# Kernel tuning notes

Hardware: AMD Instinct MI355X
Metric: run time of the kernel (lower is better)

Reference implementation:

```python
import math
import jax, jax.numpy as jnp
import numpy as np

DIM = 2048
NUM_HEADS = 16
HEAD_DIM = 128
SEQ = 2048
BATCH = 2
HIDDEN = 5632  # round_up(int(4*2048*2/3), 256)
EPS = 1e-6


def setup_inputs() -> dict:
    key = jax.random.key(0)
    ks = jax.random.split(key, 8)
    s = 0.02
    x = jax.random.normal(ks[0], (BATCH, SEQ, DIM), jnp.float32)
    wq = jax.random.normal(ks[1], (DIM, NUM_HEADS * HEAD_DIM), jnp.float32) * s
    wk = jax.random.normal(ks[2], (DIM, NUM_HEADS * HEAD_DIM), jnp.float32) * s
    wv = jax.random.normal(ks[3], (DIM, NUM_HEADS * HEAD_DIM), jnp.float32) * s
    wo = jax.random.normal(ks[4], (NUM_HEADS * HEAD_DIM, DIM), jnp.float32) * s
    w_mlp = jax.random.normal(ks[5], (HIDDEN, DIM), jnp.float32) * s
    v_mlp = jax.random.normal(ks[6], (HIDDEN, DIM), jnp.float32) * s
    w2_mlp = jax.random.normal(ks[7], (DIM, HIDDEN), jnp.float32) * s
    norm1_w = jnp.ones((DIM,), jnp.float32)
    norm2_w = jnp.ones((DIM,), jnp.float32)
    # RoPE tables: theta_i = 10000^{-2i/head_dim}, angle[p,i] = p * theta_i
    inv_freq = 1.0 / (10000.0 ** (np.arange(0, HEAD_DIM, 2, dtype=np.float32) / HEAD_DIM))
    angles = np.arange(SEQ, dtype=np.float32)[:, None] * inv_freq[None, :]  # [S, D/2]
    freqs_cos = jnp.asarray(np.cos(angles))
    freqs_sin = jnp.asarray(np.sin(angles))
    return {"x": x, "wq": wq, "wk": wk, "wv": wv, "wo": wo,
            "w_mlp": w_mlp, "v_mlp": v_mlp, "w2_mlp": w2_mlp,
            "norm1_w": norm1_w, "norm2_w": norm2_w,
            "freqs_cos": freqs_cos, "freqs_sin": freqs_sin}


def _rope(t, cos, sin):
    # t: [B,S,H,D] -> pairs, complex multiply by (cos + i sin)
    B, S, H, D = t.shape
    t = t.reshape(B, S, H, D // 2, 2)
    x0, x1 = t[..., 0], t[..., 1]
    c = cos[None, :S, None, :]
    s = sin[None, :S, None, :]
    o0 = x0 * c - x1 * s
    o1 = x0 * s + x1 * c
    return jnp.stack([o0, o1], axis=-1).reshape(B, S, H, D)


def _rmsnorm(x, w):
    x = x * jax.lax.rsqrt(jnp.mean(x * x, axis=-1, keepdims=True) + EPS)
    return w * x


def _attention(x, wq, wk, wv, wo, cos, sin):
    B, S, _ = x.shape
    q = (x @ wq).reshape(B, S, NUM_HEADS, HEAD_DIM)
    k = (x @ wk).reshape(B, S, NUM_HEADS, HEAD_DIM)
    v = (x @ wv).reshape(B, S, NUM_HEADS, HEAD_DIM)
    q = _rope(q, cos, sin)
    k = _rope(k, cos, sin)
    scores = jnp.einsum('bqhd,bkhd->bhqk', q, k) / math.sqrt(HEAD_DIM)
    causal = jnp.tril(jnp.ones((S, S), bool))
    scores = jnp.where(causal[None, None], scores, -jnp.inf)
    probs = jax.nn.softmax(scores.astype(jnp.float32), axis=-1)
    o = jnp.einsum('bhqk,bkhd->bqhd', probs, v).reshape(B, S, NUM_HEADS * HEAD_DIM)
    return o @ wo


def _mlp(x, w, v, w2):
    return (jax.nn.silu(x @ w.T) * (x @ v.T)) @ w2.T


def reference(x, wq, wk, wv, wo, w_mlp, v_mlp, w2_mlp, norm1_w, norm2_w, freqs_cos, freqs_sin):
    x = x + _attention(x, wq, wk, wv, wo, freqs_cos, freqs_sin)
    x = _rmsnorm(x, norm1_w)
    x = x + _mlp(x, w_mlp, v_mlp, w2_mlp)
    x = _rmsnorm(x, norm2_w)
    return x
```

## Files before the change

### kernel.cpp

```cpp
#include <hip/hip_runtime.h>

typedef unsigned short u16;
typedef unsigned int u32;
typedef float f32x4 __attribute__((ext_vector_type(4)));
typedef short bf16x8 __attribute__((ext_vector_type(8)));

#define DIM 2048
#define SEQ 2048
#define NHEAD 16
#define HDIM 128
#define BATCH 2
#define HIDDEN 5632
#define ROWS 4096

__device__ __forceinline__ float b2f(u16 h) { return __uint_as_float(((u32)h) << 16); }
__device__ __forceinline__ u16 f2b(float f) {
  u32 u = __float_as_uint(f);
  return (u16)((u + 0x7fffu + ((u >> 16) & 1u)) >> 16);
}

__global__ __launch_bounds__(256) void cvt_f2b(const float* __restrict__ in, u16* __restrict__ out, int n) {
  int i = (blockIdx.x * 256 + threadIdx.x) * 4;
  if (i < n) {
    float4 v = *(const float4*)(in + i);
    u32 p0 = (u32)f2b(v.x) | ((u32)f2b(v.y) << 16);
    u32 p1 = (u32)f2b(v.z) | ((u32)f2b(v.w) << 16);
    *(uint2*)(out + i) = make_uint2(p0, p1);
  }
}

__global__ __launch_bounds__(256) void cvtT(const float* __restrict__ in, u16* __restrict__ out,
                                            int Rr, int Cc) {
  __shared__ float t[32][33];
  int tx = threadIdx.x & 31, ty = threadIdx.x >> 5;
  int r0 = blockIdx.y * 32, c0 = blockIdx.x * 32;
#pragma unroll
  for (int rr = 0; rr < 4; ++rr)
    t[ty + rr * 8][tx] = in[(size_t)(r0 + ty + rr * 8) * Cc + c0 + tx];
  __syncthreads();
#pragma unroll
  for (int rr = 0; rr < 4; ++rr)
    out[(size_t)(c0 + ty + rr * 8) * Rr + r0 + tx] = f2b(t[tx][ty + rr * 8]);
}

__device__ __forceinline__ void stage_tile(u16* lds, const u16* __restrict__ g,
                                           int row0, int col0, int ld, int wave, int lane) {
#pragma unroll
  for (int j = 0; j < 2; ++j) {
    int i = wave * 2 + j;
    const u16* gp = g + (size_t)(row0 + i * 16 + (lane >> 2)) * ld + col0 + (lane & 3) * 8;
    __builtin_amdgcn_global_load_lds((const __attribute__((address_space(1))) void*)gp,
                                     (__attribute__((address_space(3))) void*)(lds + i * 512),
                                     16, 0, 0);
  }
}

template <int EPI>
__global__ __launch_bounds__(256) void gemm_bt(const u16* __restrict__ A, const u16* __restrict__ Bt,
                                               const void* R_, void* C_, int M, int N, int K) {
  __shared__ u16 lA[2][4096];
  __shared__ u16 lB[2][4096];
  const int tid = threadIdx.x, lane = tid & 63, wave = tid >> 6;
  const int wm = wave >> 1, wn = wave & 1;
  const int m0 = blockIdx.y * 128, n0 = blockIdx.x * 128;
  const int rl = lane & 15, g = lane >> 4;

  stage_tile(lA[0], A, m0, 0, K, wave, lane);
  stage_tile(lB[0], Bt, n0, 0, K, wave, lane);

  f32x4 acc[4][4];
#pragma unroll
  for (int a = 0; a < 4; ++a)
#pragma unroll
    for (int b = 0; b < 4; ++b) acc[a][b] = (f32x4){0.f, 0.f, 0.f, 0.f};

  __syncthreads();

  const int nk = K / 32;
  for (int kt = 0; kt < nk; ++kt) {
    const int cur = kt & 1;
    if (kt + 1 < nk) {
      stage_tile(lA[cur ^ 1], A, m0, (kt + 1) * 32, K, wave, lane);
      stage_tile(lB[cur ^ 1], Bt, n0, (kt + 1) * 32, K, wave, lane);
    }
    bf16x8 af[4], bfr[4];
#pragma unroll
    for (int mi = 0; mi < 4; ++mi)
      af[mi] = *reinterpret_cast<const bf16x8*>(&lA[cur][(wm * 64 + mi * 16 + rl) * 32 + g * 8]);
#pragma unroll
    for (int ni = 0; ni < 4; ++ni)
      bfr[ni] = *reinterpret_cast<const bf16x8*>(&lB[cur][(wn * 64 + ni * 16 + rl) * 32 + g * 8]);
#pragma unroll
    for (int mi = 0; mi < 4; ++mi)
#pragma unroll
      for (int ni = 0; ni < 4; ++ni)
        acc[mi][ni] = __builtin_amdgcn_mfma_f32_16x16x32_bf16(af[mi], bfr[ni], acc[mi][ni], 0, 0, 0);
    __syncthreads();
  }

#pragma unroll
  for (int mi = 0; mi < 4; ++mi)
#pragma unroll
    for (int ni = 0; ni < 4; ++ni)
#pragma unroll
      for (int j = 0; j < 4; ++j) {
        size_t row = m0 + wm * 64 + mi * 16 + g * 4 + j;
        size_t col = n0 + wn * 64 + ni * 16 + rl;
        size_t idx = row * N + col;
        float v = acc[mi][ni][j];
        if (EPI == 0) {
          ((u16*)C_)[idx] = f2b(v);
        } else if (EPI == 1) {
          ((float*)C_)[idx] = v + ((const float*)R_)[idx];
        } else if (EPI == 2) {
          float av = b2f(((const u16*)R_)[idx]);
          ((u16*)C_)[idx] = f2b(v * av / (1.f + __expf(-av)));
        } else {
          ((float*)C_)[idx] = v + b2f(((const u16*)R_)[idx]);
        }
      }
}

__global__ __launch_bounds__(256) void vtrans(const u16* __restrict__ V, u16* __restrict__ Vt) {
  __shared__ u16 t[32][33];
  int tx = threadIdx.x & 31, ty = threadIdx.x >> 5;
  int s0 = blockIdx.x * 32, d0 = blockIdx.y * 32;
  int bh = blockIdx.z, b = bh >> 4, h = bh & 15;
#pragma unroll
  for (int rr = 0; rr < 4; ++rr)
    t[ty + rr * 8][tx] = V[(size_t)(b * SEQ + s0 + ty + rr * 8) * DIM + h * HDIM + d0 + tx];
  __syncthreads();
#pragma unroll
  for (int rr = 0; rr < 4; ++rr)
    Vt[(size_t)(bh * HDIM + d0 + ty + rr * 8) * SEQ + s0 + tx] = t[tx][ty + rr * 8];
}

__global__ __launch_bounds__(256) void rope_kernel(u16* __restrict__ Q, u16* __restrict__ Kv,
                                                   const float* __restrict__ Cz, const float* __restrict__ Sz) {
  int t = blockIdx.x * 256 + threadIdx.x;
  int i = t & 63;
  int hh = (t >> 6) & 15;
  int row = t >> 10;
  int s = row & (SEQ - 1);
  float c = Cz[s * 64 + i], sn = Sz[s * 64 + i];
  size_t off = (size_t)row * DIM + hh * HDIM + 2 * i;
  const float sc = 0.08838834764831843f;

  u32 qp = *(const u32*)(Q + off);
  float q0 = b2f((u16)qp), q1 = b2f((u16)(qp >> 16));
  float o0 = (q0 * c - q1 * sn) * sc, o1 = (q0 * sn + q1 * c) * sc;
  *(u32*)(Q + off) = (u32)f2b(o0) | ((u32)f2b(o1) << 16);

  u32 kp = *(const u32*)(Kv + off);
  float k0 = b2f((u16)kp), k1 = b2f((u16)(kp >> 16));
  o0 = k0 * c - k1 * sn; o1 = k0 * sn + k1 * c;
  *(u32*)(Kv + off) = (u32)f2b(o0) | ((u32)f2b(o1) << 16);
}

__device__ __forceinline__ void attn_stage(u16* lk, u16* lv, const u16* __restrict__ Kg,
                                           const u16* __restrict__ Vg, int b, int h, int bh,
                                           int t, int w, int lane) {
#pragma unroll
  for (int j = 0; j < 4; ++j) {
    const u16* gp = Kg + (size_t)(b * SEQ + t * 64 + j * 16 + (lane >> 2)) * DIM +
                    h * HDIM + w * 32 + (lane & 3) * 8;
    __builtin_amdgcn_global_load_lds((const __attribute__((address_space(1))) void*)gp,
                                     (__attribute__((address_space(3))) void*)(lk + w * 2048 + j * 512),
                                     16, 0, 0);
  }
#pragma unroll
  for (int j = 0; j < 4; ++j) {
    int id = w * 4 + j, kc2 = id >> 3, rg = id & 7;
    const u16* gp = Vg + (size_t)(bh * HDIM + rg * 16 + (lane >> 2)) * SEQ +
                    t * 64 + kc2 * 32 + (lane & 3) * 8;
    __builtin_amdgcn_global_load_lds((const __attribute__((address_space(1))) void*)gp,
                                     (__attribute__((address_space(3))) void*)(lv + kc2 * 4096 + rg * 512),
                                     16, 0, 0);
  }
}

__device__ __forceinline__ void attn_tile(const bf16x8* qf, float* m, float* l, f32x4* oacc,
                                          int qg0, int t, bool diag,
                                          const u16* lk, const u16* lv, u16 (*pl)[72],
                                          int rl, int g) {
  f32x4 s[4];
#pragma unroll
  for (int ct = 0; ct < 4; ++ct) s[ct] = (f32x4){0.f, 0.f, 0.f, 0.f};
#pragma unroll
  for (int ct = 0; ct < 4; ++ct)
#pragma unroll
    for (int kc = 0; kc < 4; ++kc) {
      bf16x8 kf = *reinterpret_cast<const bf16x8*>(&lk[kc * 2048 + (ct * 16 + rl) * 32 + g * 8]);
      s[ct] = __builtin_amdgcn_mfma_f32_16x16x32_bf16(qf[kc], kf, s[ct], 0, 0, 0);
    }
  if (diag) {
#pragma unroll
    for (int ct = 0; ct < 4; ++ct) {
      int kg = t * 64 + ct * 16 + rl;
#pragma unroll
      for (int j = 0; j < 4; ++j)
        if (kg > qg0 + j) s[ct][j] = -1e30f;
    }
  }
  float mx[4], al[4];
#pragma unroll
  for (int j = 0; j < 4; ++j)
    mx[j] = fmaxf(fmaxf(s[0][j], s[1][j]), fmaxf(s[2][j], s[3][j]));
#pragma unroll
  for (int off = 1; off < 16; off <<= 1)
#pragma unroll
    for (int j = 0; j < 4; ++j) mx[j] = fmaxf(mx[j], __shfl_xor(mx[j], off));
#pragma unroll
  for (int j = 0; j < 4; ++j) {
    float mn = fmaxf(m[j], mx[j]);
    al[j] = __expf(m[j] - mn);
    m[j] = mn;
  }
  float rs[4] = {0.f, 0.f, 0.f, 0.f};
#pragma unroll
  for (int ct = 0; ct < 4; ++ct)
#pragma unroll
    for (int j = 0; j < 4; ++j) {
      float p = __expf(s[ct][j] - m[j]);
      s[ct][j] = p;
      rs[j] += p;
    }
#pragma unroll
  for (int off = 1; off < 16; off <<= 1)
#pragma unroll
    for (int j = 0; j < 4; ++j) rs[j] += __shfl_xor(rs[j], off);
#pragma unroll
  for (int j = 0; j < 4; ++j) l[j] = l[j] * al[j] + rs[j];
#pragma unroll
  for (int dt = 0; dt < 8; ++dt)
#pragma unroll
    for (int j = 0; j < 4; ++j) oacc[dt][j] *= al[j];

#pragma unroll
  for (int ct = 0; ct < 4; ++ct)
#pragma unroll
    for (int j = 0; j < 4; ++j) pl[g * 4 + j][ct * 16 + rl] = f2b(s[ct][j]);

  bf16x8 pa[2];
#pragma unroll
  for (int kc2 = 0; kc2 < 2; ++kc2)
    pa[kc2] = *reinterpret_cast<const bf16x8*>(&pl[rl][kc2 * 32 + g * 8]);

#pragma unroll
  for (int dt = 0; dt < 8; ++dt)
#pragma unroll
    for (int kc2 = 0; kc2 < 2; ++kc2) {
      bf16x8 vf = *reinterpret_cast<const bf16x8*>(&lv[kc2 * 4096 + (dt * 16 + rl) * 32 + g * 8]);
      oacc[dt] = __builtin_amdgcn_mfma_f32_16x16x32_bf16(pa[kc2], vf, oacc[dt], 0, 0, 0);
    }
}

__global__ __launch_bounds__(256) void attn_kernel(const u16* __restrict__ Q, const u16* __restrict__ Kp,
                                                   const u16* __restrict__ Vt, u16* __restrict__ O) {
  const int lane = threadIdx.x & 63;
  const int w = threadIdx.x >> 6;
  const int qa = blockIdx.x;
  const int qb = 31 - qa;
  const int bh = blockIdx.y;
  const int b = bh >> 4, h = bh & 15;
  const int rl = lane & 15, g = lane >> 4;

  __shared__ u16 lK[2][8192];
  __shared__ u16 lV[2][8192];
  __shared__ u16 plds[4][16][72];

  const size_t qrowA = (size_t)b * SEQ + qa * 64 + w * 16;
  const size_t qrowB = (size_t)b * SEQ + qb * 64 + w * 16;
  bf16x8 qfA[4], qfB[4];
#pragma unroll
  for (int kc = 0; kc < 4; ++kc) {
    qfA[kc] = *reinterpret_cast<const bf16x8*>(Q + (qrowA + rl) * DIM + h * HDIM + kc * 32 + g * 8);
    qfB[kc] = *reinterpret_cast<const bf16x8*>(Q + (qrowB + rl) * DIM + h * HDIM + kc * 32 + g * 8);
  }

  float mA[4], lA_[4], mB[4], lB_[4];
  f32x4 oA[8], oB[8];
#pragma unroll
  for (int j = 0; j < 4; ++j) { mA[j] = -1e30f; lA_[j] = 0.f; mB[j] = -1e30f; lB_[j] = 0.f; }
#pragma unroll
  for (int dt = 0; dt < 8; ++dt) { oA[dt] = (f32x4){0.f, 0.f, 0.f, 0.f}; oB[dt] = (f32x4){0.f, 0.f, 0.f, 0.f}; }

  const int qg0A = qa * 64 + w * 16 + g * 4;
  const int qg0B = qb * 64 + w * 16 + g * 4;

  attn_stage(lK[0], lV[0], Kp, Vt, b, h, bh, 0, w, lane);
  __syncthreads();

  int buf = 0;
  for (int t = 0; t <= qb; ++t) {
    if (t < qb) attn_stage(lK[buf ^ 1], lV[buf ^ 1], Kp, Vt, b, h, bh, t + 1, w, lane);
    attn_tile(qfB, mB, lB_, oB, qg0B, t, t == qb, lK[buf], lV[buf], plds[w], rl, g);
    if (t <= qa)
      attn_tile(qfA, mA, lA_, oA, qg0A, t, t == qa, lK[buf], lV[buf], plds[w], rl, g);
    __syncthreads();
    buf ^= 1;
  }

  float invA[4], invB[4];
#pragma unroll
  for (int j = 0; j < 4; ++j) { invA[j] = 1.f / lA_[j]; invB[j] = 1.f / lB_[j]; }
#pragma unroll
  for (int dt = 0; dt < 8; ++dt)
#pragma unroll
    for (int j = 0; j < 4; ++j) {
      O[(qrowA + g * 4 + j) * DIM + h * HDIM + dt * 16 + rl] = f2b(oA[dt][j] * invA[j]);
      O[(qrowB + g * 4 + j) * DIM + h * HDIM + dt * 16 + rl] = f2b(oB[dt][j] * invB[j]);
    }
}

__global__ __launch_bounds__(256) void rmsnorm_to_bf16(const float* __restrict__ X, const float* __restrict__ W,
                                                       u16* __restrict__ O) {
  int row = blockIdx.x, tid = threadIdx.x;
  const float* xr = X + (size_t)row * DIM + tid * 8;
  float4 a = *(const float4*)xr;
  float4 bq = *(const float4*)(xr + 4);
  float v[8] = {a.x, a.y, a.z, a.w, bq.x, bq.y, bq.z, bq.w};
  float ss = 0.f;
#pragma unroll
  for (int j = 0; j < 8; ++j) ss += v[j] * v[j];
#pragma unroll
  for (int off = 32; off; off >>= 1) ss += __shfl_xor(ss, off);
  __shared__ float wss[4];
  int wave = tid >> 6, lane = tid & 63;
  if (lane == 0) wss[wave] = ss;
  __syncthreads();
  float r = rsqrtf((wss[0] + wss[1] + wss[2] + wss[3]) * (1.f / DIM) + 1e-6f);
  float4 wa = *(const float4*)(W + tid * 8);
  float4 wb = *(const float4*)(W + tid * 8 + 4);
  float wv[8] = {wa.x, wa.y, wa.z, wa.w, wb.x, wb.y, wb.z, wb.w};
  uint4 ou;
  ou.x = (u32)f2b(v[0] * r * wv[0]) | ((u32)f2b(v[1] * r * wv[1]) << 16);
  ou.y = (u32)f2b(v[2] * r * wv[2]) | ((u32)f2b(v[3] * r * wv[3]) << 16);
  ou.z = (u32)f2b(v[4] * r * wv[4]) | ((u32)f2b(v[5] * r * wv[5]) << 16);
  ou.w = (u32)f2b(v[6] * r * wv[6]) | ((u32)f2b(v[7] * r * wv[7]) << 16);
  *(uint4*)(O + (size_t)row * DIM + tid * 8) = ou;
}

__global__ __launch_bounds__(256) void rmsnorm_to_f32(const float* __restrict__ X, const float* __restrict__ W,
                                                      float* __restrict__ O) {
  int row = blockIdx.x, tid = threadIdx.x;
  const float* xr = X + (size_t)row * DIM + tid * 8;
  float4 a = *(const float4*)xr;
  float4 bq = *(const float4*)(xr + 4);
  float v[8] = {a.x, a.y, a.z, a.w, bq.x, bq.y, bq.z, bq.w};
  float ss = 0.f;
#pragma unroll
  for (int j = 0; j < 8; ++j) ss += v[j] * v[j];
#pragma unroll
  for (int off = 32; off; off >>= 1) ss += __shfl_xor(ss, off);
  __shared__ float wss[4];
  int wave = tid >> 6, lane = tid & 63;
  if (lane == 0) wss[wave] = ss;
  __syncthreads();
  float r = rsqrtf((wss[0] + wss[1] + wss[2] + wss[3]) * (1.f / DIM) + 1e-6f);
  float4 wa = *(const float4*)(W + tid * 8);
  float4 wb = *(const float4*)(W + tid * 8 + 4);
  float wv[8] = {wa.x, wa.y, wa.z, wa.w, wb.x, wb.y, wb.z, wb.w};
  float4 o0 = {v[0] * r * wv[0], v[1] * r * wv[1], v[2] * r * wv[2], v[3] * r * wv[3]};
  float4 o1 = {v[4] * r * wv[4], v[5] * r * wv[5], v[6] * r * wv[6], v[7] * r * wv[7]};
  *(float4*)(O + (size_t)row * DIM + tid * 8) = o0;
  *(float4*)(O + (size_t)row * DIM + tid * 8 + 4) = o1;
}

extern "C" void kernel_launch(void* const* d_in, const int* in_sizes, int n_in,
                              void* d_out, int out_size, void* d_ws, size_t ws_size,
                              hipStream_t stream) {
  const float* x     = (const float*)d_in[0];
  const float* wq    = (const float*)d_in[1];
  const float* wk    = (const float*)d_in[2];
  const float* wv    = (const float*)d_in[3];
  const float* wo    = (const float*)d_in[4];
  const float* w_mlp = (const float*)d_in[5];
  const float* v_mlp = (const float*)d_in[6];
  const float* w2    = (const float*)d_in[7];
  const float* n1w   = (const float*)d_in[8];
  const float* n2w   = (const float*)d_in[9];
  const float* fcos  = (const float*)d_in[10];
  const float* fsin  = (const float*)d_in[11];

  u16* ws = (u16*)d_ws;
  const size_t SZ = (size_t)ROWS * DIM;
  const size_t DD = (size_t)DIM * DIM;
  const size_t DH = (size_t)DIM * HIDDEN;

  u16* xb  = ws;
  u16* q   = ws + SZ;
  u16* k   = ws + 2 * SZ;
  u16* v   = ws + 3 * SZ;
  u16* vt  = ws + 4 * SZ;
  u16* hb  = ws + 5 * SZ;
  u16* W   = ws + 6 * SZ;
  u16* wqT = W;
  u16* wkT = W + DD;
  u16* wvT = W + 2 * DD;
  u16* woT = W + 3 * DD;
  u16* wmb = W;
  u16* vmb = W + DH;
  u16* w2b = W;
  float* x1f = (float*)ws;
  float* x2f = (float*)ws;
  u16* ba  = ws + 2 * SZ;

  dim3 blk(256);

  cvt_f2b<<<(int)(SZ / 4 / 256), blk, 0, stream>>>(x, xb, (int)SZ);
  dim3 gT(DIM / 32, DIM / 32);
  cvtT<<<gT, blk, 0, stream>>>(wq, wqT, DIM, DIM);
  cvtT<<<gT, blk, 0, stream>>>(wk, wkT, DIM, DIM);
  cvtT<<<gT, blk, 0, stream>>>(wv, wvT, DIM, DIM);
  cvtT<<<gT, blk, 0, stream>>>(wo, woT, DIM, DIM);

  dim3 gP(DIM / 128, ROWS / 128);
  gemm_bt<0><<<gP, blk, 0, stream>>>(xb, wqT, nullptr, q, ROWS, DIM, DIM);
  gemm_bt<0><<<gP, blk, 0, stream>>>(xb, wkT, nullptr, k, ROWS, DIM, DIM);
  gemm_bt<0><<<gP, blk, 0, stream>>>(xb, wvT, nullptr, v, ROWS, DIM, DIM);

  cvt_f2b<<<(int)(DH / 4 / 256), blk, 0, stream>>>(w_mlp, wmb, (int)DH);

  rope_kernel<<<(ROWS * NHEAD * 64) / 256, blk, 0, stream>>>(q, k, fcos, fsin);
  vtrans<<<dim3(SEQ / 32, HDIM / 32, BATCH * NHEAD), blk, 0, stream>>>(v, vt);

  attn_kernel<<<dim3(16, BATCH * NHEAD), blk, 0, stream>>>(q, k, vt, v);

  gemm_bt<1><<<gP, blk, 0, stream>>>(v, woT, x, x1f, ROWS, DIM, DIM);

  cvt_f2b<<<(int)(DH / 4 / 256), blk, 0, stream>>>(v_mlp, vmb, (int)DH);

  rmsnorm_to_bf16<<<ROWS, blk, 0, stream>>>(x1f, n1w, hb);

  dim3 gM1(HIDDEN / 128, ROWS / 128);
  gemm_bt<0><<<gM1, blk, 0, stream>>>(hb, wmb, nullptr, ba, ROWS, HIDDEN, DIM);
  gemm_bt<2><<<gM1, blk, 0, stream>>>(hb, vmb, ba, ba, ROWS, HIDDEN, DIM);

  cvt_f2b<<<(int)(DH / 4 / 256), blk, 0, stream>>>(w2, w2b, (int)DH);

  gemm_bt<3><<<gP, blk, 0, stream>>>(ba, w2b, hb, x2f, ROWS, DIM, HIDDEN);
  rmsnorm_to_f32<<<ROWS, blk, 0, stream>>>(x2f, n2w, (float*)d_out);
}
```

Baseline: 879.3 us.

## Fuse QKV GEMMs, swizzle workgroup order, XOR-swizzle attention LDS, finer barriers

Merges the three Q/K/V projection GEMMs into one launch over the concatenated transposed weights, with a new epilogue that scatters the output columns into the separate q/k/v buffers. Remaps workgroup IDs in both GEMM and attention so consecutive blocks land on different XCDs, for better L2 locality. XOR-swizzles the K/V tile placement in LDS to cut bank conflicts, and replaces __syncthreads with explicit vmcnt/lgkmcnt waits plus raw barriers so the next tile's loads can stay in flight. The swizzles rely on the grid being divisible by 8 and on the concatenated weight layout holding in the workspace.

```diff
diff --git a/kernel.cpp b/kernel.cpp
--- a/kernel.cpp
+++ b/kernel.cpp
@@ -62,7 +62,12 @@
   __shared__ u16 lB[2][4096];
   const int tid = threadIdx.x, lane = tid & 63, wave = tid >> 6;
   const int wm = wave >> 1, wn = wave & 1;
-  const int m0 = blockIdx.y * 128, n0 = blockIdx.x * 128;
+  const int gx = gridDim.x;
+  const int nwg = gx * gridDim.y;
+  const int id = blockIdx.y * gx + blockIdx.x;
+  const int cpx = nwg >> 3;
+  const int sw = (id & 7) * cpx + (id >> 3);
+  const int m0 = (sw / gx) * 128, n0 = (sw % gx) * 128;
   const int rl = lane & 15, g = lane >> 4;
 
   stage_tile(lA[0], A, m0, 0, K, wave, lane);
@@ -115,8 +120,11 @@
         } else if (EPI == 2) {
           float av = b2f(((const u16*)R_)[idx]);
           ((u16*)C_)[idx] = f2b(v * av / (1.f + __expf(-av)));
+        } else if (EPI == 3) {
+          ((float*)C_)[idx] = v + b2f(((const u16*)R_)[idx]);
         } else {
-          ((float*)C_)[idx] = v + b2f(((const u16*)R_)[idx]);
+          size_t di = (col >> 11) * (size_t)(ROWS * (size_t)DIM) + row * DIM + (col & (DIM - 1));
+          ((u16*)C_)[di] = f2b(v);
         }
       }
 }
@@ -160,10 +168,12 @@
 __device__ __forceinline__ void attn_stage(u16* lk, u16* lv, const u16* __restrict__ Kg,
                                            const u16* __restrict__ Vg, int b, int h, int bh,
                                            int t, int w, int lane) {
+  const int r4 = lane >> 2;
+  const int gsw = (lane & 3) ^ (r4 & 3);
 #pragma unroll
   for (int j = 0; j < 4; ++j) {
-    const u16* gp = Kg + (size_t)(b * SEQ + t * 64 + j * 16 + (lane >> 2)) * DIM +
-                    h * HDIM + w * 32 + (lane & 3) * 8;
+    const u16* gp = Kg + (size_t)(b * SEQ + t * 64 + j * 16 + r4) * DIM +
+                    h * HDIM + w * 32 + gsw * 8;
     __builtin_amdgcn_global_load_lds((const __attribute__((address_space(1))) void*)gp,
                                      (__attribute__((address_space(3))) void*)(lk + w * 2048 + j * 512),
                                      16, 0, 0);
@@ -171,8 +181,8 @@
 #pragma unroll
   for (int j = 0; j < 4; ++j) {
     int id = w * 4 + j, kc2 = id >> 3, rg = id & 7;
-    const u16* gp = Vg + (size_t)(bh * HDIM + rg * 16 + (lane >> 2)) * SEQ +
-                    t * 64 + kc2 * 32 + (lane & 3) * 8;
+    const u16* gp = Vg + (size_t)(bh * HDIM + rg * 16 + r4) * SEQ +
+                    t * 64 + kc2 * 32 + gsw * 8;
     __builtin_amdgcn_global_load_lds((const __attribute__((address_space(1))) void*)gp,
                                      (__attribute__((address_space(3))) void*)(lv + kc2 * 4096 + rg * 512),
                                      16, 0, 0);
@@ -183,6 +193,7 @@
                                           int qg0, int t, bool diag,
                                           const u16* lk, const u16* lv, u16 (*pl)[72],
                                           int rl, int g) {
+  const int gx8 = (g ^ (rl & 3)) * 8;
   f32x4 s[4];
 #pragma unroll
   for (int ct = 0; ct < 4; ++ct) s[ct] = (f32x4){0.f, 0.f, 0.f, 0.f};
@@ -190,7 +201,7 @@
   for (int ct = 0; ct < 4; ++ct)
 #pragma unroll
     for (int kc = 0; kc < 4; ++kc) {
-      bf16x8 kf = *reinterpret_cast<const bf16x8*>(&lk[kc * 2048 + (ct * 16 + rl) * 32 + g * 8]);
+      bf16x8 kf = *reinterpret_cast<const bf16x8*>(&lk[kc * 2048 + (ct * 16 + rl) * 32 + gx8]);
       s[ct] = __builtin_amdgcn_mfma_f32_16x16x32_bf16(qf[kc], kf, s[ct], 0, 0, 0);
     }
   if (diag) {
@@ -250,7 +261,7 @@
   for (int dt = 0; dt < 8; ++dt)
 #pragma unroll
     for (int kc2 = 0; kc2 < 2; ++kc2) {
-      bf16x8 vf = *reinterpret_cast<const bf16x8*>(&lv[kc2 * 4096 + (dt * 16 + rl) * 32 + g * 8]);
+      bf16x8 vf = *reinterpret_cast<const bf16x8*>(&lv[kc2 * 4096 + (dt * 16 + rl) * 32 + gx8]);
       oacc[dt] = __builtin_amdgcn_mfma_f32_16x16x32_bf16(pa[kc2], vf, oacc[dt], 0, 0, 0);
     }
 }
@@ -259,9 +270,11 @@
                                                    const u16* __restrict__ Vt, u16* __restrict__ O) {
   const int lane = threadIdx.x & 63;
   const int w = threadIdx.x >> 6;
-  const int qa = blockIdx.x;
+  const int id = blockIdx.y * 16 + blockIdx.x;
+  const int sw = (id & 7) * 64 + (id >> 3);
+  const int qa = sw & 15;
   const int qb = 31 - qa;
-  const int bh = blockIdx.y;
+  const int bh = sw >> 4;
   const int b = bh >> 4, h = bh & 15;
   const int rl = lane & 15, g = lane >> 4;
 
@@ -289,15 +302,23 @@
   const int qg0B = qb * 64 + w * 16 + g * 4;
 
   attn_stage(lK[0], lV[0], Kp, Vt, b, h, bh, 0, w, lane);
-  __syncthreads();
 
   int buf = 0;
   for (int t = 0; t <= qb; ++t) {
-    if (t < qb) attn_stage(lK[buf ^ 1], lV[buf ^ 1], Kp, Vt, b, h, bh, t + 1, w, lane);
+    if (t < qb) {
+      attn_stage(lK[buf ^ 1], lV[buf ^ 1], Kp, Vt, b, h, bh, t + 1, w, lane);
+      asm volatile("s_waitcnt vmcnt(8)" ::: "memory");
+    } else {
+      asm volatile("s_waitcnt vmcnt(0)" ::: "memory");
+    }
+    __builtin_amdgcn_s_barrier();
+    __builtin_amdgcn_sched_barrier(0);
     attn_tile(qfB, mB, lB_, oB, qg0B, t, t == qb, lK[buf], lV[buf], plds[w], rl, g);
     if (t <= qa)
       attn_tile(qfA, mA, lA_, oA, qg0A, t, t == qa, lK[buf], lV[buf], plds[w], rl, g);
-    __syncthreads();
+    asm volatile("s_waitcnt lgkmcnt(0)" ::: "memory");
+    __builtin_amdgcn_sched_barrier(0);
+    __builtin_amdgcn_s_barrier();
     buf ^= 1;
   }
 
@@ -415,10 +436,8 @@
   cvtT<<<gT, blk, 0, stream>>>(wv, wvT, DIM, DIM);
   cvtT<<<gT, blk, 0, stream>>>(wo, woT, DIM, DIM);
 
-  dim3 gP(DIM / 128, ROWS / 128);
-  gemm_bt<0><<<gP, blk, 0, stream>>>(xb, wqT, nullptr, q, ROWS, DIM, DIM);
-  gemm_bt<0><<<gP, blk, 0, stream>>>(xb, wkT, nullptr, k, ROWS, DIM, DIM);
-  gemm_bt<0><<<gP, blk, 0, stream>>>(xb, wvT, nullptr, v, ROWS, DIM, DIM);
+  dim3 gQKV(3 * DIM / 128, ROWS / 128);
+  gemm_bt<4><<<gQKV, blk, 0, stream>>>(xb, W, nullptr, q, ROWS, 3 * DIM, DIM);
 
   cvt_f2b<<<(int)(DH / 4 / 256), blk, 0, stream>>>(w_mlp, wmb, (int)DH);
 
@@ -427,6 +446,7 @@
 
   attn_kernel<<<dim3(16, BATCH * NHEAD), blk, 0, stream>>>(q, k, vt, v);
 
+  dim3 gP(DIM / 128, ROWS / 128);
   gemm_bt<1><<<gP, blk, 0, stream>>>(v, woT, x, x1f, ROWS, DIM, DIM);
 
   cvt_f2b<<<(int)(DH / 4 / 256), blk, 0, stream>>>(v_mlp, vmb, (int)DH);
```

After: 842.7 us. 4.2% less time.
